# Kernel tuning notes

Measured on AMD Instinct MI355X. Metric: run time of the kernel, lower is better.

## Reference

```python
import jax, jax.numpy as jnp
import numpy as np

EPS_RMS = 1e-8
EPS_LN = 1e-5


def _rms(x):
    return x / jnp.sqrt(jnp.mean(x * x, axis=-1, keepdims=True) + EPS_RMS)


def _ln(x, g, b):
    m = jnp.mean(x, axis=-1, keepdims=True)
    v = jnp.mean((x - m) ** 2, axis=-1, keepdims=True)
    return (x - m) / jnp.sqrt(v + EPS_LN) * g + b


def setup_inputs() -> dict:
    B, S, D, K, V, F = 2, 256, 1024, 8, 32000, 2048
    key = jax.random.key(0)
    ks = jax.random.split(key, 12)
    s = 0.02

    def n(k, shape):
        return jax.random.normal(k, shape, dtype=jnp.float32) * s

    return {
        "x": jax.random.randint(ks[0], (B, S), 0, V),
        "embed_table": n(ks[1], (V, D)),
        "unembed_w": n(ks[2], (V, D)),
        "proj_w": n(ks[3], (K, D, 2 * D)),
        "proj_b": jnp.zeros((K, D), jnp.float32),
        "sa_wv": n(ks[4], (K, D, D)),
        "sa_bv": jnp.zeros((K, D), jnp.float32),
        "sa_wo": n(ks[5], (K, D, D)),
        "sa_bo": jnp.zeros((K, D), jnp.float32),
        "ln1_g": jnp.ones((K, D), jnp.float32),
        "ln1_b": jnp.zeros((K, D), jnp.float32),
        "ca_wv": n(ks[6], (K, D, D)),
        "ca_bv": jnp.zeros((K, D), jnp.float32),
        "ca_wo": n(ks[7], (K, D, D)),
        "ca_bo": jnp.zeros((K, D), jnp.float32),
        "ln2_g": jnp.ones((K, D), jnp.float32),
        "ln2_b": jnp.zeros((K, D), jnp.float32),
        "ff_w1": n(ks[8], (K, F, D)),
        "ff_b1": jnp.zeros((K, F), jnp.float32),
        "ff_w2": n(ks[9], (K, D, F)),
        "ff_b2": jnp.zeros((K, D), jnp.float32),
        "ln3_g": jnp.ones((K, D), jnp.float32),
        "ln3_b": jnp.zeros((K, D), jnp.float32),
    }


def reference(x, embed_table, unembed_w, proj_w, proj_b,
              sa_wv, sa_bv, sa_wo, sa_bo, ln1_g, ln1_b,
              ca_wv, ca_bv, ca_wo, ca_bo, ln2_g, ln2_b,
              ff_w1, ff_b1, ff_w2, ff_b2, ln3_g, ln3_b):
    K = proj_w.shape[0]
    emb = embed_table[x]                      # [B, S, D]
    B, S, D = emb.shape
    I = S - K                                 # number of outer positions (max_i + 1)
    h = emb[:, :I, :]                         # h_prev for all start positions, [B, I, D]
    logits_k = []
    for k in range(K):
        e = emb[:, k + 1:k + 1 + I, :]        # future token embeds for head k
        merged = jnp.concatenate([_rms(h), _rms(e)], axis=-1)   # [B, I, 2D]
        xp = jnp.einsum('bid,ed->bie', merged, proj_w[k]) + proj_b[k]
        # TransformerDecoderLayer on a length-1 sequence: softmax over a single
        # key == 1, so (self-/cross-)attention reduces to out_proj(v_proj(.)).
        sa = (xp @ sa_wv[k].T + sa_bv[k]) @ sa_wo[k].T + sa_bo[k]
        x1 = _ln(xp + sa, ln1_g[k], ln1_b[k])
        ca = (xp @ ca_wv[k].T + ca_bv[k]) @ ca_wo[k].T + ca_bo[k]   # memory = layer input
        x2 = _ln(x1 + ca, ln2_g[k], ln2_b[k])
        ff = jax.nn.relu(x2 @ ff_w1[k].T + ff_b1[k]) @ ff_w2[k].T + ff_b2[k]
        x3 = _ln(x2 + ff, ln3_g[k], ln3_b[k])
        logits_k.append(x3 @ unembed_w.T)     # [B, I, V]
        h = x3
    return jnp.stack(logits_k, axis=2)        # [B, I, K, V]
```

## Files before the change

### kernel.cpp

```cpp
#include <hip/hip_runtime.h>
#include <hip/hip_bf16.h>

#define Dd 1024
#define Ss 256
#define Bz 2
#define Kk 8
#define Vv 32000
#define Ff 2048
#define Ii 248
#define Mm (Bz*Ii)
#define Mp 512
#define Mu (Kk*Mm)
#define Mx 4096

typedef __attribute__((ext_vector_type(8))) short bf16x8_t;
typedef __attribute__((ext_vector_type(4))) float f32x4_t;
typedef unsigned long long u64;

__device__ inline ushort f2b(float f) {
    union { float f; unsigned u; } v; v.f = f;
    unsigned u = v.u;
    unsigned r = (u + 0x7fffu + ((u >> 16) & 1u)) >> 16;
    return (ushort)r;
}

__device__ inline void gload16(const void* g, void* l) {
    __builtin_amdgcn_global_load_lds((const __attribute__((address_space(1))) void*)g,
                                     (__attribute__((address_space(3))) void*)l, 16, 0, 0);
}

template<int N> __device__ inline void wait_vmcnt() {
    asm volatile("s_waitcnt vmcnt(%0)" :: "n"(N) : "memory");
}
__device__ inline void bar() {
    asm volatile("" ::: "memory");
    __builtin_amdgcn_s_barrier();
    asm volatile("" ::: "memory");
}

template<int BK>
__device__ inline int swz(int s, int r) {
    if constexpr (BK == 64) return s ^ (r & 7);
    else                    return s ^ ((r >> 1) & 3);
}

template<int BM, int BN, int BK, int TH, int PF, bool RELU, bool UNEMBED>
__global__ __launch_bounds__(TH, 2)
void gemm3(const ushort* __restrict__ A0, const ushort* __restrict__ A1, int lda,
           const ushort* __restrict__ W0, const ushort* __restrict__ W1,
           const float* __restrict__ b0, const float* __restrict__ b1,
           float* __restrict__ Cf0, float* __restrict__ Cf1,
           ushort* __restrict__ Cb0, ushort* __restrict__ Cb1,
           int Mrows, int N, int KDIM) {
    constexpr int NW = TH / 64;
    constexpr int WN = NW / 2;
    constexpr int MR = (BM / 2) / 16;
    constexpr int NR = (BN / WN) / 16;
    constexpr int TILE = (BM + BN) * BK;
    constexpr int ABYTES = BM * BK * 2;
    constexpr int TOT = (BM + BN) * BK * 2;
    constexpr int L = TOT / (TH * 16);
    constexpr int KS = BK / 32;

    __shared__ __align__(16) ushort sm[PF * TILE];

    const ushort* A = A0; const ushort* W = W0; const float* bias = b0;
    float* Cf = Cf0; ushort* Cb = Cb0;
    if (blockIdx.z) { A = A1; W = W1; bias = b1; Cf = Cf1; Cb = Cb1; }

    int bx = blockIdx.x, by = blockIdx.y;
    if constexpr (UNEMBED) {
        const int nwg  = gridDim.x * gridDim.y;
        const int orig = by * gridDim.x + bx;
        const int q = nwg >> 3, r = nwg & 7;
        const int xcd = orig & 7, lin = orig >> 3;
        const int wg = (xcd < r ? xcd * (q + 1) : r * (q + 1) + (xcd - r) * q) + lin;
        bx = wg % gridDim.x; by = wg / gridDim.x;
    }

    const int t    = threadIdx.x;
    const int tm0  = bx * BM;
    const int tn0  = by * BN;
    const int lane = t & 63;
    const int w    = t >> 6;
    const int wr   = (w / WN) * (BM / 2);
    const int wc   = (w % WN) * (BN / WN);

    const ushort* Abase = A + (size_t)tm0 * lda;
    const ushort* Wbase = W + (size_t)tn0 * KDIM;

    const ushort* gp[L];
    int lo[L];
    #pragma unroll
    for (int j = 0; j < L; ++j) {
        const int i = (t + j * TH) * 16;
        int r, s; const ushort* base; int ld;
        if (i < ABYTES) { r = i / (BK * 2); s = (i >> 4) % (BK / 8); base = Abase; ld = lda; }
        else { const int i2 = i - ABYTES; r = i2 / (BK * 2); s = (i2 >> 4) % (BK / 8); base = Wbase; ld = KDIM; }
        gp[j] = base + (size_t)r * ld + swz<BK>(s, r) * 8;
        lo[j] = i / 2;
    }
    auto stage = [&](int buf) {
        #pragma unroll
        for (int j = 0; j < L; ++j) gload16(gp[j], &sm[buf * TILE + lo[j]]);
        #pragma unroll
        for (int j = 0; j < L; ++j) gp[j] += BK;
    };

    const int h = lane >> 4, rl = lane & 15;
    int aoff[MR][KS], boff[NR][KS];
    #pragma unroll
    for (int m = 0; m < MR; ++m)
        #pragma unroll
        for (int kk = 0; kk < KS; ++kk) {
            const int r = wr + m * 16 + rl;
            aoff[m][kk] = r * BK + swz<BK>(kk * 4 + h, r) * 8;
        }
    #pragma unroll
    for (int n = 0; n < NR; ++n)
        #pragma unroll
        for (int kk = 0; kk < KS; ++kk) {
            const int r = wc + n * 16 + rl;
            boff[n][kk] = BM * BK + r * BK + swz<BK>(kk * 4 + h, r) * 8;
        }

    f32x4_t acc[MR][NR] = {};

    const int NT = KDIM / BK;
    #pragma unroll
    for (int p = 0; p < PF; ++p) stage(p);

    int buf = 0;
    for (int kt = 0; kt < NT; ++kt) {
        const int remT = NT - 1 - kt;
        const int wv = remT < PF - 1 ? remT : PF - 1;
        switch (wv) {
            case 0:  wait_vmcnt<0>();     break;
            case 1:  wait_vmcnt<1 * L>(); break;
            case 2:  wait_vmcnt<2 * L>(); break;
            default: wait_vmcnt<3 * L>(); break;
        }
        bar();

        const ushort* smb = &sm[buf * TILE];
        #pragma unroll
        for (int kk = 0; kk < KS; ++kk) {
            bf16x8_t af[MR], bf[NR];
            #pragma unroll
            for (int m = 0; m < MR; ++m) af[m] = *(const bf16x8_t*)&smb[aoff[m][kk]];
            #pragma unroll
            for (int n = 0; n < NR; ++n) bf[n] = *(const bf16x8_t*)&smb[boff[n][kk]];
            #pragma unroll
            for (int m = 0; m < MR; ++m)
                #pragma unroll
                for (int n = 0; n < NR; ++n)
                    acc[m][n] = __builtin_amdgcn_mfma_f32_16x16x32_bf16(af[m], bf[n], acc[m][n], 0, 0, 0);
        }
        bar();
        if (kt + PF < NT) stage(buf);
        buf = (buf + 1 == PF) ? 0 : buf + 1;
    }

    const int rb = (lane >> 4) * 4;
    const int cl = lane & 15;
    #pragma unroll
    for (int m = 0; m < MR; ++m)
        #pragma unroll
        for (int n = 0; n < NR; ++n)
            #pragma unroll
            for (int i = 0; i < 4; ++i) {
                const int r = tm0 + wr + m * 16 + rb + i;
                const int c = tn0 + wc + n * 16 + cl;
                if (r < Mrows) {
                    float v = acc[m][n][i];
                    if (bias) v += bias[c];
                    if (RELU) v = fmaxf(v, 0.f);
                    if (UNEMBED) {
                        const int kk  = r / Mm;
                        const int rem = r - kk * Mm;
                        Cf[(size_t)(rem * Kk + kk) * Vv + c] = v;
                    } else {
                        if (Cf) Cf[(size_t)r * N + c] = v;
                        if (Cb) Cb[(size_t)r * N + c] = f2b(v);
                    }
                }
            }
}

__global__ __launch_bounds__(256)
void convert_k(const float* __restrict__ src, ushort* __restrict__ dst,
               long n, long perK, long dstPerK, long dstOff) {
    long i = ((long)blockIdx.x * 256 + threadIdx.x) * 4;
    const long stride = (long)gridDim.x * 1024;
    for (; i < n; i += stride) {
        const float4 v = *(const float4*)(src + i);
        const long k = i / perK, rem = i - k * perK;
        ushort4 hh; hh.x = f2b(v.x); hh.y = f2b(v.y); hh.z = f2b(v.z); hh.w = f2b(v.w);
        *(ushort4*)(dst + k * dstPerK + dstOff + rem) = hh;
    }
}

__global__ __launch_bounds__(256)
void copyf_k(const float* __restrict__ src, float* __restrict__ dst,
             long n, long perK, long dstPerK, long dstOff) {
    long i = (long)blockIdx.x * 256 + threadIdx.x;
    const long stride = (long)gridDim.x * 256;
    for (; i < n; i += stride) {
        const long k = i / perK, rem = i - k * perK;
        dst[k * dstPerK + dstOff + rem] = src[i];
    }
}


__global__ __launch_bounds__(256)
void ln12_kernel(const float* __restrict__ sa, const float* __restrict__ xp,
                 const float* __restrict__ ca,
                 const float* __restrict__ g1, const float* __restrict__ b1,
                 const float* __restrict__ g2, const float* __restrict__ b2,
                 float* __restrict__ x2f, ushort* __restrict__ x2b) {
    __shared__ float reds[16];
    const int row = blockIdx.x;
    const int t = threadIdx.x;
    const float4 va = *(const float4*)(sa + (size_t)row * Dd + t * 4);
    const float4 vp = *(const float4*)(xp + (size_t)row * Dd + t * 4);
    float x[4] = { va.x + vp.x, va.y + vp.y, va.z + vp.z, va.w + vp.w };
    float s = x[0] + x[1] + x[2] + x[3];
    float q = x[0]*x[0] + x[1]*x[1] + x[2]*x[2] + x[3]*x[3];
    for (int m = 32; m; m >>= 1) { s += __shfl_xor(s, m); q += __shfl_xor(q, m); }
    if ((t & 63) == 0) { reds[t >> 6] = s; reds[4 + (t >> 6)] = q; }
    __syncthreads();
    s = reds[0] + reds[1] + reds[2] + reds[3];
    q = reds[4] + reds[5] + reds[6] + reds[7];
    float mean = s * (1.f / Dd);
    float rstd = rsqrtf(q * (1.f / Dd) - mean * mean + 1e-5f);
    const float4 vc = *(const float4*)(ca + (size_t)row * Dd + t * 4);
    float y[4];
    #pragma unroll
    for (int j = 0; j < 4; ++j) {
        const int c = t * 4 + j;
        y[j] = (x[j] - mean) * rstd * g1[c] + b1[c] + ((const float*)&vc)[j];
    }
    s = y[0] + y[1] + y[2] + y[3];
    q = y[0]*y[0] + y[1]*y[1] + y[2]*y[2] + y[3]*y[3];
    for (int m = 32; m; m >>= 1) { s += __shfl_xor(s, m); q += __shfl_xor(q, m); }
    if ((t & 63) == 0) { reds[8 + (t >> 6)] = s; reds[12 + (t >> 6)] = q; }
    __syncthreads();
    s = reds[8] + reds[9] + reds[10] + reds[11];
    q = reds[12] + reds[13] + reds[14] + reds[15];
    mean = s * (1.f / Dd);
    rstd = rsqrtf(q * (1.f / Dd) - mean * mean + 1e-5f);
    float z[4]; ushort4 hb;
    #pragma unroll
    for (int j = 0; j < 4; ++j) {
        const int c = t * 4 + j;
        z[j] = (y[j] - mean) * rstd * g2[c] + b2[c];
    }
    hb.x = f2b(z[0]); hb.y = f2b(z[1]); hb.z = f2b(z[2]); hb.w = f2b(z[3]);
    *(float4*)(x2f + (size_t)row * Dd + t * 4) = make_float4(z[0], z[1], z[2], z[3]);
    *(ushort4*)(x2b + (size_t)row * Dd + t * 4) = hb;
}

__global__ __launch_bounds__(256)
void ln3m_kernel(const float* __restrict__ ff, const float* __restrict__ x2,
                 const float* __restrict__ g3, const float* __restrict__ b3,
                 const ushort* __restrict__ remb, ushort* __restrict__ x3k,
                 ushort* __restrict__ merged, int k) {
    __shared__ float reds[12];
    const int r = blockIdx.x;
    const int t = threadIdx.x;
    const int b = r / Ii, i = r - b * Ii;
    const float4 vf = *(const float4*)(ff + (size_t)r * Dd + t * 4);
    const float4 v2 = *(const float4*)(x2 + (size_t)r * Dd + t * 4);
    float x[4] = { vf.x + v2.x, vf.y + v2.y, vf.z + v2.z, vf.w + v2.w };
    float s = x[0] + x[1] + x[2] + x[3];
    float q = x[0]*x[0] + x[1]*x[1] + x[2]*x[2] + x[3]*x[3];
    for (int m = 32; m; m >>= 1) { s += __shfl_xor(s, m); q += __shfl_xor(q, m); }
    if ((t & 63) == 0) { reds[t >> 6] = s; reds[4 + (t >> 6)] = q; }
    __syncthreads();
    s = reds[0] + reds[1] + reds[2] + reds[3];
    q = reds[4] + reds[5] + reds[6] + reds[7];
    const float mean = s * (1.f / Dd);
    const float rstd = rsqrtf(q * (1.f / Dd) - mean * mean + 1e-5f);
    float y[4];
    #pragma unroll
    for (int j = 0; j < 4; ++j) {
        const int c = t * 4 + j;
        y[j] = (x[j] - mean) * rstd * g3[c] + b3[c];
    }
    ushort4 hy; hy.x = f2b(y[0]); hy.y = f2b(y[1]); hy.z = f2b(y[2]); hy.w = f2b(y[3]);
    *(ushort4*)(x3k + (size_t)r * Dd + t * 4) = hy;
    float q2 = y[0]*y[0] + y[1]*y[1] + y[2]*y[2] + y[3]*y[3];
    for (int m = 32; m; m >>= 1) q2 += __shfl_xor(q2, m);
    if ((t & 63) == 0) reds[8 + (t >> 6)] = q2;
    __syncthreads();
    if (k + 1 < Kk) {
        q2 = reds[8] + reds[9] + reds[10] + reds[11];
        const float sc = rsqrtf(q2 * (1.f / Dd) + 1e-8f);
        ushort4 hm; hm.x = f2b(y[0]*sc); hm.y = f2b(y[1]*sc); hm.z = f2b(y[2]*sc); hm.w = f2b(y[3]*sc);
        *(ushort4*)(merged + (size_t)r * (2 * Dd) + t * 4) = hm;
        const ushort4 ev = *(const ushort4*)(remb + (size_t)(b * Ss + k + 2 + i) * Dd + t * 4);
        *(ushort4*)(merged + (size_t)r * (2 * Dd) + Dd + t * 4) = ev;
    }
}

__global__ __launch_bounds__(256)
void gather_rms_merged(const int* __restrict__ xi, const float* __restrict__ table,
                       ushort* __restrict__ remb, ushort* __restrict__ merged) {
    __shared__ float reds[4];
    const int row = blockIdx.x;
    const int t = threadIdx.x;
    const int idx = xi[row];
    const float4 xv = *(const float4*)(table + (size_t)idx * Dd + t * 4);
    float q = xv.x*xv.x + xv.y*xv.y + xv.z*xv.z + xv.w*xv.w;
    for (int m = 32; m; m >>= 1) q += __shfl_xor(q, m);
    if ((t & 63) == 0) reds[t >> 6] = q;
    __syncthreads();
    q = reds[0] + reds[1] + reds[2] + reds[3];
    const float sc = rsqrtf(q * (1.f / Dd) + 1e-8f);
    ushort4 h;
    h.x = f2b(xv.x * sc); h.y = f2b(xv.y * sc); h.z = f2b(xv.z * sc); h.w = f2b(xv.w * sc);
    *(ushort4*)(remb + (size_t)row * Dd + t * 4) = h;
    const int b = row / Ss, s2 = row - b * Ss;
    if (s2 < Ii)
        *(ushort4*)(merged + (size_t)(b * Ii + s2) * (2 * Dd) + t * 4) = h;
    if (s2 >= 1 && s2 <= Ii)
        *(ushort4*)(merged + (size_t)(b * Ii + s2 - 1) * (2 * Dd) + Dd + t * 4) = h;
}


__device__ inline bf16x8_t ld_frag(const ushort* p) {
    union { u64 l[2]; bf16x8_t s; } u;
    u.l[0] = *(const u64*)p;
    u.l[1] = *(const u64*)(p + 4);
    return u.s;
}

#define LDST 40

template<int KDIM, bool RELU, bool UNEMBED>
__global__ __launch_bounds__(256)
void gemm64(const ushort* __restrict__ A, const float* __restrict__ Wt,
            const float* __restrict__ bias, float* __restrict__ Cf,
            ushort* __restrict__ Cb, int Mrows, int N) {
    __shared__ ushort As[64 * LDST];
    __shared__ ushort Ws[64 * LDST];
    const int t    = threadIdx.x;
    const int tm0  = blockIdx.x * 64;
    const int tn0  = blockIdx.y * 64;
    const int lr   = t >> 2;
    const int lc   = (t & 3) * 8;
    const int wid  = t >> 6;
    const int lane = t & 63;
    const int wr   = (wid >> 1) * 32;
    const int wc   = (wid & 1) * 32;
    f32x4_t acc[2][2] = {};
    const bool avalid = (tm0 + lr) < Mrows;
    const ushort* Ap = A  + (size_t)(tm0 + lr) * KDIM + lc;
    const float*  Wp = Wt + (size_t)(tn0 + lr) * KDIM + lc;
    const int aoff = lr * LDST + lc;

    for (int k0 = 0; k0 < KDIM; k0 += 32) {
        union { uint4 qv; u64 l[2]; } av;
        av.qv = make_uint4(0u, 0u, 0u, 0u);
        if (avalid) av.qv = *(const uint4*)(Ap + k0);
        const float4 w0 = *(const float4*)(Wp + k0);
        const float4 w1 = *(const float4*)(Wp + k0 + 4);
        union { ushort us[8]; u64 l[2]; } wb;
        wb.us[0] = f2b(w0.x); wb.us[1] = f2b(w0.y); wb.us[2] = f2b(w0.z); wb.us[3] = f2b(w0.w);
        wb.us[4] = f2b(w1.x); wb.us[5] = f2b(w1.y); wb.us[6] = f2b(w1.z); wb.us[7] = f2b(w1.w);
        __syncthreads();
        *(u64*)&As[aoff]     = av.l[0];
        *(u64*)&As[aoff + 4] = av.l[1];
        *(u64*)&Ws[aoff]     = wb.l[0];
        *(u64*)&Ws[aoff + 4] = wb.l[1];
        __syncthreads();

        const ushort* ab = &As[(wr + (lane & 15)) * LDST + (lane >> 4) * 8];
        const ushort* bb = &Ws[(wc + (lane & 15)) * LDST + (lane >> 4) * 8];
        const bf16x8_t fa0 = ld_frag(ab);
        const bf16x8_t fa1 = ld_frag(ab + 16 * LDST);
        const bf16x8_t fb0 = ld_frag(bb);
        const bf16x8_t fb1 = ld_frag(bb + 16 * LDST);
        acc[0][0] = __builtin_amdgcn_mfma_f32_16x16x32_bf16(fa0, fb0, acc[0][0], 0, 0, 0);
        acc[0][1] = __builtin_amdgcn_mfma_f32_16x16x32_bf16(fa0, fb1, acc[0][1], 0, 0, 0);
        acc[1][0] = __builtin_amdgcn_mfma_f32_16x16x32_bf16(fa1, fb0, acc[1][0], 0, 0, 0);
        acc[1][1] = __builtin_amdgcn_mfma_f32_16x16x32_bf16(fa1, fb1, acc[1][1], 0, 0, 0);
    }

    const int rb = (lane >> 4) * 4;
    const int cl = lane & 15;
    for (int m = 0; m < 2; ++m)
        for (int n = 0; n < 2; ++n)
            for (int i = 0; i < 4; ++i) {
                const int r = tm0 + wr + m * 16 + rb + i;
                const int c = tn0 + wc + n * 16 + cl;
                if (r < Mrows) {
                    float v = acc[m][n][i];
                    if (bias) v += bias[c];
                    if (RELU) v = fmaxf(v, 0.f);
                    if (UNEMBED) {
                        const int kk  = r / Mm;
                        const int rem = r - kk * Mm;
                        Cf[(size_t)(rem * Kk + kk) * Vv + c] = v;
                    } else {
                        if (Cf) Cf[(size_t)r * N + c] = v;
                        if (Cb) Cb[(size_t)r * N + c] = f2b(v);
                    }
                }
            }
}

__global__ __launch_bounds__(256)
void ln_kernel(const float* __restrict__ a, const float* __restrict__ rsd,
               const float* __restrict__ g, const float* __restrict__ bb,
               float* __restrict__ outf, ushort* __restrict__ outb) {
    __shared__ float reds[8];
    const int row = blockIdx.x;
    const int t = threadIdx.x;
    const float4 xa = *(const float4*)(a   + (size_t)row * Dd + t * 4);
    const float4 xr = *(const float4*)(rsd + (size_t)row * Dd + t * 4);
    float x[4] = { xa.x + xr.x, xa.y + xr.y, xa.z + xr.z, xa.w + xr.w };
    float s = x[0] + x[1] + x[2] + x[3];
    float q = x[0]*x[0] + x[1]*x[1] + x[2]*x[2] + x[3]*x[3];
    for (int msk = 32; msk; msk >>= 1) { s += __shfl_xor(s, msk); q += __shfl_xor(q, msk); }
    if ((t & 63) == 0) { reds[t >> 6] = s; reds[4 + (t >> 6)] = q; }
    __syncthreads();
    s = reds[0] + reds[1] + reds[2] + reds[3];
    q = reds[4] + reds[5] + reds[6] + reds[7];
    const float m    = s * (1.f / Dd);
    const float var  = q * (1.f / Dd) - m * m;
    const float rstd = rsqrtf(var + 1e-5f);
    float y[4];
    #pragma unroll
    for (int j = 0; j < 4; ++j) {
        const int c = t * 4 + j;
        y[j] = (x[j] - m) * rstd * g[c] + bb[c];
    }
    if (outf) *(float4*)(outf + (size_t)row * Dd + t * 4) = make_float4(y[0], y[1], y[2], y[3]);
    if (outb) {
        ushort4 h; h.x = f2b(y[0]); h.y = f2b(y[1]); h.z = f2b(y[2]); h.w = f2b(y[3]);
        *(ushort4*)(outb + (size_t)row * Dd + t * 4) = h;
    }
}

__global__ __launch_bounds__(256)
void build_merged(const float* __restrict__ h, const ushort* __restrict__ remb,
                  ushort* __restrict__ merged, int k) {
    __shared__ float reds[4];
    const int r = blockIdx.x;
    const int t = threadIdx.x;
    const int b = r / Ii;
    const int i = r - b * Ii;
    if (k == 0) {
        const ushort4 hv = *(const ushort4*)(remb + (size_t)(b * Ss + i) * Dd + t * 4);
        *(ushort4*)(merged + (size_t)r * (2 * Dd) + t * 4) = hv;
    } else {
        const float4 xv = *(const float4*)(h + (size_t)r * Dd + t * 4);
        float q = xv.x*xv.x + xv.y*xv.y + xv.z*xv.z + xv.w*xv.w;
        for (int msk = 32; msk; msk >>= 1) q += __shfl_xor(q, msk);
        if ((t & 63) == 0) reds[t >> 6] = q;
        __syncthreads();
        q = reds[0] + reds[1] + reds[2] + reds[3];
        const float sc = rsqrtf(q * (1.f / Dd) + 1e-8f);
        ushort4 hv;
        hv.x = f2b(xv.x * sc); hv.y = f2b(xv.y * sc); hv.z = f2b(xv.z * sc); hv.w = f2b(xv.w * sc);
        *(ushort4*)(merged + (size_t)r * (2 * Dd) + t * 4) = hv;
    }
    const ushort4 ev = *(const ushort4*)(remb + (size_t)(b * Ss + k + 1 + i) * Dd + t * 4);
    *(ushort4*)(merged + (size_t)r * (2 * Dd) + Dd + t * 4) = ev;
}

__global__ __launch_bounds__(256)
void gather_rms(const int* __restrict__ xi, const float* __restrict__ table,
                ushort* __restrict__ remb) {
    __shared__ float reds[4];
    const int row = blockIdx.x;
    const int t = threadIdx.x;
    const int idx = xi[row];
    const float4 xv = *(const float4*)(table + (size_t)idx * Dd + t * 4);
    float q = xv.x*xv.x + xv.y*xv.y + xv.z*xv.z + xv.w*xv.w;
    for (int msk = 32; msk; msk >>= 1) q += __shfl_xor(q, msk);
    if ((t & 63) == 0) reds[t >> 6] = q;
    __syncthreads();
    q = reds[0] + reds[1] + reds[2] + reds[3];
    const float sc = rsqrtf(q * (1.f / Dd) + 1e-8f);
    ushort4 h;
    h.x = f2b(xv.x * sc); h.y = f2b(xv.y * sc); h.z = f2b(xv.z * sc); h.w = f2b(xv.w * sc);
    *(ushort4*)(remb + (size_t)row * Dd + t * 4) = h;
}


extern "C" void kernel_launch(void* const* d_in, const int* in_sizes, int n_in,
                              void* d_out, int out_size, void* d_ws, size_t ws_size,
                              hipStream_t stream) {
    const int*   x      = (const int*)  d_in[0];
    const float* table  = (const float*)d_in[1];
    const float* unemb  = (const float*)d_in[2];
    const float* proj_w = (const float*)d_in[3];
    const float* proj_b = (const float*)d_in[4];
    const float* sa_wv  = (const float*)d_in[5];
    const float* sa_bv  = (const float*)d_in[6];
    const float* sa_wo  = (const float*)d_in[7];
    const float* sa_bo  = (const float*)d_in[8];
    const float* ln1_g  = (const float*)d_in[9];
    const float* ln1_b  = (const float*)d_in[10];
    const float* ca_wv  = (const float*)d_in[11];
    const float* ca_bv  = (const float*)d_in[12];
    const float* ca_wo  = (const float*)d_in[13];
    const float* ca_bo  = (const float*)d_in[14];
    const float* ln2_g  = (const float*)d_in[15];
    const float* ln2_b  = (const float*)d_in[16];
    const float* ff_w1  = (const float*)d_in[17];
    const float* ff_b1  = (const float*)d_in[18];
    const float* ff_w2  = (const float*)d_in[19];
    const float* ff_b2  = (const float*)d_in[20];
    const float* ln3_g  = (const float*)d_in[21];
    const float* ln3_b  = (const float*)d_in[22];
    float* out = (float*)d_out;

    char* ws = (char*)d_ws;
    size_t off = 0;
    auto alloc = [&](size_t bytes) -> void* {
        void* p = ws + off;
        off = (off + bytes + 255) & ~(size_t)255;
        return p;
    };

    const size_t NEED = 262100000;

    if (ws_size >= NEED) {
        ushort* wU  = (ushort*)alloc((size_t)Vv * Dd * 2);
        ushort* wP  = (ushort*)alloc((size_t)Kk * Dd * 2 * Dd * 2);
        ushort* wV  = (ushort*)alloc((size_t)Kk * 2 * Dd * Dd * 2);
        ushort* wOs = (ushort*)alloc((size_t)Kk * Dd * Dd * 2);
        ushort* wOc = (ushort*)alloc((size_t)Kk * Dd * Dd * 2);
        ushort* wF1 = (ushort*)alloc((size_t)Kk * Ff * Dd * 2);
        ushort* wF2 = (ushort*)alloc((size_t)Kk * Dd * Ff * 2);
        float*  bV  = (float*) alloc((size_t)Kk * 2 * Dd * 4);
        ushort* remb   = (ushort*)alloc((size_t)Bz * Ss * Dd * 2);
        ushort* merged = (ushort*)alloc((size_t)Mp * 2 * Dd * 2);
        float*  xpf    = (float*) alloc((size_t)Mp * Dd * 4);
        ushort* xpb    = (ushort*)alloc((size_t)Mp * Dd * 2);
        ushort* tb     = (ushort*)alloc((size_t)Mp * 2 * Dd * 2);
        float*  sfa    = (float*) alloc((size_t)Mp * Dd * 4);
        float*  sfc    = (float*) alloc((size_t)Mp * Dd * 4);
        float*  x2f    = (float*) alloc((size_t)Mp * Dd * 4);
        ushort* x2b    = (ushort*)alloc((size_t)Mp * Dd * 2);
        ushort* x3all  = (ushort*)alloc((size_t)Mx * Dd * 2);

        const long nU = (long)Vv * Dd;
        convert_k<<<2048, 256, 0, stream>>>(unemb, wU, nU, nU, nU, 0);
        const long nP = (long)Kk * Dd * 2 * Dd;
        convert_k<<<2048, 256, 0, stream>>>(proj_w, wP, nP, nP, nP, 0);
        const long nDD = (long)Kk * Dd * Dd, pDD = (long)Dd * Dd, pV = 2 * pDD;
        convert_k<<<2048, 256, 0, stream>>>(sa_wv, wV, nDD, pDD, pV, 0);
        convert_k<<<2048, 256, 0, stream>>>(ca_wv, wV, nDD, pDD, pV, pDD);
        convert_k<<<2048, 256, 0, stream>>>(sa_wo, wOs, nDD, nDD, nDD, 0);
        convert_k<<<2048, 256, 0, stream>>>(ca_wo, wOc, nDD, nDD, nDD, 0);
        const long nF = (long)Kk * Ff * Dd;
        convert_k<<<2048, 256, 0, stream>>>(ff_w1, wF1, nF, nF, nF, 0);
        convert_k<<<2048, 256, 0, stream>>>(ff_w2, wF2, nF, nF, nF, 0);
        copyf_k<<<32, 256, 0, stream>>>(sa_bv, bV, (long)Kk * Dd, Dd, 2 * Dd, 0);
        copyf_k<<<32, 256, 0, stream>>>(ca_bv, bV, (long)Kk * Dd, Dd, 2 * Dd, Dd);

        gather_rms_merged<<<Bz * Ss, 256, 0, stream>>>(x, table, remb, merged);

        for (int k = 0; k < Kk; ++k) {
            gemm3<32, 64, 64, 256, 3, false, false><<<dim3(Mp/32, Dd/64, 1), 256, 0, stream>>>(
                merged, merged, 2 * Dd, wP + (size_t)k * Dd * 2 * Dd, wP + (size_t)k * Dd * 2 * Dd,
                proj_b + k * Dd, proj_b + k * Dd, xpf, xpf, xpb, xpb, Mm, Dd, 2 * Dd);
            gemm3<32, 64, 64, 256, 3, false, false><<<dim3(Mp/32, 2*Dd/64, 1), 256, 0, stream>>>(
                xpb, xpb, Dd, wV + (size_t)k * pV, wV + (size_t)k * pV,
                bV + (size_t)k * 2 * Dd, bV + (size_t)k * 2 * Dd,
                nullptr, nullptr, tb, tb, Mm, 2 * Dd, Dd);
            gemm3<32, 64, 64, 256, 3, false, false><<<dim3(Mp/32, Dd/64, 2), 256, 0, stream>>>(
                tb, tb + Dd, 2 * Dd, wOs + (size_t)k * pDD, wOc + (size_t)k * pDD,
                sa_bo + k * Dd, ca_bo + k * Dd, sfa, sfc, nullptr, nullptr, Mm, Dd, Dd);
            ln12_kernel<<<Mm, 256, 0, stream>>>(sfa, xpf, sfc,
                ln1_g + k * Dd, ln1_b + k * Dd, ln2_g + k * Dd, ln2_b + k * Dd, x2f, x2b);
            gemm3<32, 64, 64, 256, 3, true, false><<<dim3(Mp/32, Ff/64, 1), 256, 0, stream>>>(
                x2b, x2b, Dd, wF1 + (size_t)k * Ff * Dd, wF1 + (size_t)k * Ff * Dd,
                ff_b1 + k * Ff, ff_b1 + k * Ff, nullptr, nullptr, tb, tb, Mm, Ff, Dd);
            gemm3<32, 64, 64, 256, 3, false, false><<<dim3(Mp/32, Dd/64, 1), 256, 0, stream>>>(
                tb, tb, Ff, wF2 + (size_t)k * Dd * Ff, wF2 + (size_t)k * Dd * Ff,
                ff_b2 + k * Dd, ff_b2 + k * Dd, sfa, sfa, nullptr, nullptr, Mm, Dd, Ff);
            ln3m_kernel<<<Mm, 256, 0, stream>>>(sfa, x2f, ln3_g + k * Dd, ln3_b + k * Dd,
                remb, x3all + (size_t)k * Mm * Dd, merged, k);
        }

        gemm3<256, 256, 64, 512, 2, false, true><<<dim3(Mx/256, Vv/256, 1), 512, 0, stream>>>(
            x3all, x3all, Dd, wU, wU, nullptr, nullptr, out, out, nullptr, nullptr, Mu, Vv, Dd);
        return;
    }

    ushort* remb   = (ushort*)alloc((size_t)Bz * Ss * Dd * 2);
    ushort* merged = (ushort*)alloc((size_t)Mm * 2 * Dd * 2);
    float*  xpf    = (float*) alloc((size_t)Mm * Dd * 4);
    ushort* xpb    = (ushort*)alloc((size_t)Mm * Dd * 2);
    ushort* tb     = (ushort*)alloc((size_t)Mm * Ff * 2);
    float*  sf     = (float*) alloc((size_t)Mm * Dd * 4);
    float*  x1f    = (float*) alloc((size_t)Mm * Dd * 4);
    float*  x2f    = (float*) alloc((size_t)Mm * Dd * 4);
    ushort* x2b    = (ushort*)alloc((size_t)Mm * Dd * 2);
    float*  hbuf   = (float*) alloc((size_t)Mm * Dd * 4);
    ushort* x3all  = (ushort*)alloc((size_t)Kk * Mm * Dd * 2);

    gather_rms<<<Bz * Ss, 256, 0, stream>>>(x, table, remb);

    const dim3 gD((Mm + 63) / 64, Dd / 64);
    const dim3 gF((Mm + 63) / 64, Ff / 64);
    for (int k = 0; k < Kk; ++k) {
        build_merged<<<Mm, 256, 0, stream>>>(hbuf, remb, merged, k);
        gemm64<2 * Dd, false, false><<<gD, 256, 0, stream>>>(
            merged, proj_w + (size_t)k * Dd * 2 * Dd, proj_b + k * Dd, xpf, xpb, Mm, Dd);
        gemm64<Dd, false, false><<<gD, 256, 0, stream>>>(
            xpb, sa_wv + (size_t)k * Dd * Dd, sa_bv + k * Dd, nullptr, tb, Mm, Dd);
        gemm64<Dd, false, false><<<gD, 256, 0, stream>>>(
            tb, sa_wo + (size_t)k * Dd * Dd, sa_bo + k * Dd, sf, nullptr, Mm, Dd);
        ln_kernel<<<Mm, 256, 0, stream>>>(sf, xpf, ln1_g + k * Dd, ln1_b + k * Dd, x1f, nullptr);
        gemm64<Dd, false, false><<<gD, 256, 0, stream>>>(
            xpb, ca_wv + (size_t)k * Dd * Dd, ca_bv + k * Dd, nullptr, tb, Mm, Dd);
        gemm64<Dd, false, false><<<gD, 256, 0, stream>>>(
            tb, ca_wo + (size_t)k * Dd * Dd, ca_bo + k * Dd, sf, nullptr, Mm, Dd);
        ln_kernel<<<Mm, 256, 0, stream>>>(sf, x1f, ln2_g + k * Dd, ln2_b + k * Dd, x2f, x2b);
        gemm64<Dd, true, false><<<gF, 256, 0, stream>>>(
            x2b, ff_w1 + (size_t)k * Ff * Dd, ff_b1 + k * Ff, nullptr, tb, Mm, Ff);
        gemm64<Ff, false, false><<<gD, 256, 0, stream>>>(
            tb, ff_w2 + (size_t)k * Dd * Ff, ff_b2 + k * Dd, sf, nullptr, Mm, Dd);
        ln_kernel<<<Mm, 256, 0, stream>>>(sf, x2f, ln3_g + k * Dd, ln3_b + k * Dd,
                                          hbuf, x3all + (size_t)k * Mm * Dd);
    }

    const dim3 gU((Kk * Mm) / 64, Vv / 64);
    gemm64<Dd, false, true><<<gU, 256, 0, stream>>>(x3all, unemb, nullptr, out, nullptr, Kk * Mm, Vv);
}
```

Baseline: 988.2 us.

## Add dedicated 8-wave ping-pong unembed GEMM kernel with 4-stage LDS pipeline

```diff
diff --git a/kernel.cpp b/kernel.cpp
--- a/kernel.cpp
+++ b/kernel.cpp
@@ -32,6 +32,10 @@
 template<int N> __device__ inline void wait_vmcnt() {
     asm volatile("s_waitcnt vmcnt(%0)" :: "n"(N) : "memory");
 }
+__device__ inline void lgkm0() {
+    asm volatile("s_waitcnt lgkmcnt(0)" ::: "memory");
+    __builtin_amdgcn_sched_barrier(0);
+}
 __device__ inline void bar() {
     asm volatile("" ::: "memory");
     __builtin_amdgcn_s_barrier();
@@ -42,6 +46,127 @@
 __device__ inline int swz(int s, int r) {
     if constexpr (BK == 64) return s ^ (r & 7);
     else                    return s ^ ((r >> 1) & 3);
+}
+
+__global__ __launch_bounds__(512, 2)
+void gemm8p(const ushort* __restrict__ A, const ushort* __restrict__ W,
+            float* __restrict__ Cf, int Mrows, int KDIM) {
+    constexpr int BM = 256, BN = 256, BK = 32;
+    constexpr int TILE = (BM + BN) * BK;
+    constexpr int ABYTES = BM * BK * 2;
+    __shared__ __align__(16) ushort sm[4 * TILE];
+
+    int bx = blockIdx.x, by = blockIdx.y;
+    {
+        const int nwg  = gridDim.x * gridDim.y;
+        const int orig = by * gridDim.x + bx;
+        const int q = nwg >> 3, r = nwg & 7;
+        const int xcd = orig & 7, lin = orig >> 3;
+        const int wg = (xcd < r ? xcd * (q + 1) : r * (q + 1) + (xcd - r) * q) + lin;
+        bx = wg % gridDim.x; by = wg / gridDim.x;
+    }
+    const int t    = threadIdx.x;
+    const int lane = t & 63;
+    const int w    = t >> 6;
+    const int wr   = (w >> 2) * 128;
+    const int wc   = (w & 3) * 64;
+    const int tm0  = bx * BM, tn0 = by * BN;
+
+    const ushort* Abase = A + (size_t)tm0 * KDIM;
+    const ushort* Wbase = W + (size_t)tn0 * KDIM;
+
+    const ushort* gp[4]; int lo[4];
+    #pragma unroll
+    for (int j = 0; j < 4; ++j) {
+        const int i = (t + j * 512) * 16;
+        int r, s; const ushort* base;
+        if (i < ABYTES) { r = i / (BK * 2); s = (i >> 4) & 3; base = Abase; }
+        else { const int i2 = i - ABYTES; r = i2 / (BK * 2); s = (i2 >> 4) & 3; base = Wbase; }
+        gp[j] = base + (size_t)r * KDIM + (size_t)swz<BK>(s, r) * 8;
+        lo[j] = i / 2;
+    }
+    const int h = lane >> 4, rl = lane & 15;
+    int aoff[8], boff[4];
+    #pragma unroll
+    for (int m = 0; m < 8; ++m) { const int r = wr + m * 16 + rl; aoff[m] = r * BK + swz<BK>(h, r) * 8; }
+    #pragma unroll
+    for (int n = 0; n < 4; ++n) { const int r = wc + n * 16 + rl; boff[n] = BM * BK + r * BK + swz<BK>(h, r) * 8; }
+
+    f32x4_t acc[8][4] = {};
+    const int NT = KDIM / BK;
+
+    #pragma unroll
+    for (int p = 0; p < 3; ++p) {
+        gload16(gp[0], &sm[p * TILE + lo[0]]); gload16(gp[1], &sm[p * TILE + lo[1]]);
+        gload16(gp[2], &sm[p * TILE + lo[2]]); gload16(gp[3], &sm[p * TILE + lo[3]]);
+        gp[0] += BK; gp[1] += BK; gp[2] += BK; gp[3] += BK;
+    }
+    wait_vmcnt<8>();
+    bar();
+
+    int buf = 0;
+    for (int tt = 0; tt < NT; ++tt) {
+        const ushort* smb = &sm[buf * TILE];
+        bf16x8_t af[8], b0, b1;
+        #pragma unroll
+        for (int m = 0; m < 8; ++m) af[m] = *(const bf16x8_t*)&smb[aoff[m]];
+        b0 = *(const bf16x8_t*)&smb[boff[0]];
+        b1 = *(const bf16x8_t*)&smb[boff[1]];
+        if (tt + 3 < NT) {
+            const int db = (tt + 3) & 3;
+            gload16(gp[0], &sm[db * TILE + lo[0]]);
+            gload16(gp[1], &sm[db * TILE + lo[1]]);
+        }
+        bar();
+        lgkm0();
+        __builtin_amdgcn_s_setprio(1);
+        #pragma unroll
+        for (int m = 0; m < 8; ++m) {
+            acc[m][0] = __builtin_amdgcn_mfma_f32_16x16x32_bf16(af[m], b0, acc[m][0], 0, 0, 0);
+            acc[m][1] = __builtin_amdgcn_mfma_f32_16x16x32_bf16(af[m], b1, acc[m][1], 0, 0, 0);
+        }
+        __builtin_amdgcn_s_setprio(0);
+        bar();
+        bf16x8_t b2 = *(const bf16x8_t*)&smb[boff[2]];
+        bf16x8_t b3 = *(const bf16x8_t*)&smb[boff[3]];
+        if (tt + 3 < NT) {
+            const int db = (tt + 3) & 3;
+            gload16(gp[2], &sm[db * TILE + lo[2]]);
+            gload16(gp[3], &sm[db * TILE + lo[3]]);
+            gp[0] += BK; gp[1] += BK; gp[2] += BK; gp[3] += BK;
+        }
+        if (tt + 3 < NT)      wait_vmcnt<8>();
+        else if (tt + 2 < NT) wait_vmcnt<4>();
+        else                  wait_vmcnt<0>();
+        bar();
+        lgkm0();
+        __builtin_amdgcn_s_setprio(1);
+        #pragma unroll
+        for (int m = 0; m < 8; ++m) {
+            acc[m][2] = __builtin_amdgcn_mfma_f32_16x16x32_bf16(af[m], b2, acc[m][2], 0, 0, 0);
+            acc[m][3] = __builtin_amdgcn_mfma_f32_16x16x32_bf16(af[m], b3, acc[m][3], 0, 0, 0);
+        }
+        __builtin_amdgcn_s_setprio(0);
+        bar();
+        buf = (buf + 1) & 3;
+    }
+
+    const int rb = (lane >> 4) * 4;
+    const int cl = lane & 15;
+    #pragma unroll
+    for (int m = 0; m < 8; ++m)
+        #pragma unroll
+        for (int n = 0; n < 4; ++n)
+            #pragma unroll
+            for (int i = 0; i < 4; ++i) {
+                const int r = tm0 + wr + m * 16 + rb + i;
+                const int c = tn0 + wc + n * 16 + cl;
+                if (r < Mrows) {
+                    const int kk  = r / Mm;
+                    const int rem = r - kk * Mm;
+                    Cf[(size_t)(rem * Kk + kk) * Vv + c] = acc[m][n][i];
+                }
+            }
 }
 
 template<int BM, int BN, int BK, int TH, int PF, bool RELU, bool UNEMBED>
@@ -68,19 +193,9 @@
     float* Cf = Cf0; ushort* Cb = Cb0;
     if (blockIdx.z) { A = A1; W = W1; bias = b1; Cf = Cf1; Cb = Cb1; }
 
-    int bx = blockIdx.x, by = blockIdx.y;
-    if constexpr (UNEMBED) {
-        const int nwg  = gridDim.x * gridDim.y;
-        const int orig = by * gridDim.x + bx;
-        const int q = nwg >> 3, r = nwg & 7;
-        const int xcd = orig & 7, lin = orig >> 3;
-        const int wg = (xcd < r ? xcd * (q + 1) : r * (q + 1) + (xcd - r) * q) + lin;
-        bx = wg % gridDim.x; by = wg / gridDim.x;
-    }
-
     const int t    = threadIdx.x;
-    const int tm0  = bx * BM;
-    const int tn0  = by * BN;
+    const int tm0  = blockIdx.x * BM;
+    const int tn0  = blockIdx.y * BN;
     const int lane = t & 63;
     const int w    = t >> 6;
     const int wr   = (w / WN) * (BM / 2);
@@ -588,8 +703,7 @@
                 remb, x3all + (size_t)k * Mm * Dd, merged, k);
         }
 
-        gemm3<256, 256, 64, 512, 2, false, true><<<dim3(Mx/256, Vv/256, 1), 512, 0, stream>>>(
-            x3all, x3all, Dd, wU, wU, nullptr, nullptr, out, out, nullptr, nullptr, Mu, Vv, Dd);
+        gemm8p<<<dim3(Mx/256, Vv/256, 1), 512, 0, stream>>>(x3all, wU, out, Mu, Dd);
         return;
     }
 
```

New measurement: 996.4 us. No clear change (+0.8%).
